# Optimization experiments

Measured on AMD Instinct MI355X. Metric: run time of the kernel, lower is better.

## Reference

```python
import jax, jax.numpy as jnp
import numpy as np

N, E, B, F, H = 50000, 600000, 256, 128, 128
RATIO = 0.8
BN_EPS = 1e-5


def _topk_keep(score, batch, mask):
    # Per-graph top-ceil(RATIO*live) selection, expressed as a fixed-size keep mask.
    s = jnp.where(mask, score, -jnp.inf)
    order = jnp.lexsort((-s, batch))  # primary: batch id, secondary: score desc
    rank = jnp.zeros(N, dtype=jnp.int32).at[order].set(jnp.arange(N, dtype=jnp.int32))
    total = jax.ops.segment_sum(jnp.ones(N, dtype=jnp.int32), batch, B)
    starts = jnp.cumsum(total) - total
    r_in_g = (rank - starts[batch]).astype(jnp.float32)  # rank within own graph
    live = jax.ops.segment_sum(mask.astype(jnp.float32), batch, B)
    k = jnp.ceil(RATIO * live)
    return (r_in_g < k[batch]) & mask


def _forward(x, edge_index, batch, W1s, b1s, W2s, b2s, gammas, betas, pool_ws):
    src, dst = edge_index[0], edge_index[1]
    mask = jnp.ones(N, dtype=bool)      # live-node mask (TopK pooling shrinks graphs)
    e_mask = jnp.ones(E, dtype=bool)    # live-edge mask
    out = jnp.zeros((B, 2 * H), dtype=x.dtype)
    for i in range(4):
        # GINConv (eps=0): MLP(x + sum_{j->i} x_j)
        msg = jnp.where(e_mask[:, None], x[src], 0.0)
        agg = jax.ops.segment_sum(msg, dst, num_segments=N)
        h = x + agg
        h = jax.nn.relu(h @ W1s[i] + b1s[i]) @ W2s[i] + b2s[i]
        # BatchNorm (training mode) over live nodes only
        m = mask[:, None].astype(h.dtype)
        n = jnp.maximum(jnp.sum(m), 1.0)
        mean = jnp.sum(h * m, axis=0) / n
        var = jnp.sum(((h - mean) ** 2) * m, axis=0) / n
        h = (h - mean) * jax.lax.rsqrt(var + BN_EPS) * gammas[i] + betas[i]
        h = jax.nn.relu(h) * m
        # TopKPooling(ratio=0.8): score = x@w/||w||, keep top-k per graph, scale by tanh
        w = pool_ws[i]
        score = (h @ w) / jnp.linalg.norm(w)
        keep = _topk_keep(score, batch, mask)
        x = jnp.where(keep[:, None], h * jnp.tanh(score)[:, None], 0.0)
        mask = keep
        e_mask = e_mask & keep[src] & keep[dst]
        # global max pool + global mean pool over live nodes
        mx = jax.ops.segment_max(jnp.where(mask[:, None], x, -jnp.inf), batch, num_segments=B)
        mx = jnp.where(jnp.isfinite(mx), mx, 0.0)
        cnt = jax.ops.segment_sum(mask.astype(x.dtype), batch, num_segments=B)
        mn = jax.ops.segment_sum(x, batch, num_segments=B) / jnp.maximum(cnt, 1.0)[:, None]
        out = out + jnp.concatenate([mx, mn], axis=1)  # x1 + x2 + x3 + x4
    return out


def setup_inputs() -> dict:
    key = jax.random.key(0)
    k = jax.random.split(key, 8)
    s = 1.0 / np.sqrt(H)
    return {
        "x": jax.random.normal(k[0], (N, F), jnp.float32),
        "edge_index": jax.random.randint(k[1], (2, E), 0, N),
        "batch": jnp.sort(jax.random.randint(k[2], (N,), 0, B)),
        "W1s": jax.random.normal(k[3], (4, F, H), jnp.float32) * s,
        "b1s": jax.random.normal(k[4], (4, H), jnp.float32) * s,
        "W2s": jax.random.normal(k[5], (4, H, H), jnp.float32) * s,
        "b2s": jax.random.normal(k[6], (4, H), jnp.float32) * s,
        "gammas": jnp.ones((4, H), jnp.float32),
        "betas": jnp.zeros((4, H), jnp.float32),
        "pool_ws": jax.random.normal(k[7], (4, H), jnp.float32) * s,
    }


def reference(x, edge_index, batch, W1s, b1s, W2s, b2s, gammas, betas, pool_ws):
    return _forward(x, edge_index, batch, W1s, b1s, W2s, b2s, gammas, betas, pool_ws)
```

## Files before the change

### kernel.cpp

```cpp
#include <hip/hip_runtime.h>
#include <hip/hip_bf16.h>
#include <math.h>


#define HF 128
#define CHUNK_LG 14

typedef __attribute__((ext_vector_type(8))) short short8;
typedef __attribute__((ext_vector_type(4))) float floatx4;

__device__ __forceinline__ unsigned short cvt_bf16(float f) {
    unsigned u = __float_as_uint(f);
    u = u + 0x7fffu + ((u >> 16) & 1u);
    return (unsigned short)(u >> 16);
}
__device__ __forceinline__ float bf16f(unsigned short h) {
    return __uint_as_float(((unsigned)h) << 16);
}

__device__ __forceinline__ void split3(float f, short& p1, short& p2, short& p3) {
    unsigned u = __float_as_uint(f);
    unsigned r = u + 0x7fffu + ((u >> 16) & 1u);
    p1 = (short)(r >> 16);
    float r1 = f - __uint_as_float(r & 0xffff0000u);
    unsigned u1 = __float_as_uint(r1);
    p2 = (short)(u1 >> 16);
    float r2 = r1 - __uint_as_float(u1 & 0xffff0000u);
    p3 = (short)(__float_as_uint(r2) >> 16);
}


__global__ __launch_bounds__(256)
void k_hist(const int* __restrict__ dst, unsigned int* __restrict__ partial,
            unsigned char* __restrict__ eslot, int* __restrict__ mask,
            float* __restrict__ stats4, float* __restrict__ out,
            int* __restrict__ lc,
            int N, int E, int nd4, int outsz, int X) {
    __shared__ unsigned int lh[12544];
    int bl = blockIdx.x, tid = threadIdx.x;
    for (int i = tid; i < nd4; i += 256) lh[i] = 0;
    __syncthreads();
    int e0 = bl << CHUNK_LG;
    int e1 = min(E, e0 + (1 << CHUNK_LG));
    for (int e = e0 + tid; e < e1; e += 256) {
        int d = dst[e];
        unsigned int old = atomicAdd(&lh[d >> 2], 1u << (8 * (d & 3)));
        eslot[e] = (unsigned char)((old >> (8 * (d & 3))) & 255u);
    }
    __syncthreads();
    for (int i = tid; i < nd4; i += 256) partial[(size_t)bl * nd4 + i] = lh[i];
    int gt = bl * 256 + tid, tot = X * 256;
    for (int i = gt; i < N; i += tot) mask[i] = 1;
    for (int i = gt; i < 4 * 256; i += tot) stats4[i] = 0.f;
    for (int i = gt; i < outsz; i += tot) out[i] = 0.f;
    if (gt < 5) lc[gt] = (gt == 0) ? N : 0;
}

__global__ __launch_bounds__(256)
void k_colsum(const unsigned int* __restrict__ partial, unsigned int* __restrict__ baseoff,
              int* __restrict__ deg, int* __restrict__ blocksum,
              int nd4, int X, int N) {
    __shared__ int red[256];
    int tid = threadIdx.x;
    int d4 = blockIdx.x * 256 + tid;
    unsigned int run = 0;
    if (d4 < nd4) {
        for (int bl = 0; bl < X; ++bl) {
            unsigned int c = partial[(size_t)bl * nd4 + d4];
            baseoff[(size_t)bl * nd4 + d4] = run;
            run += c;
        }
        int d = d4 * 4;
#pragma unroll
        for (int j = 0; j < 4; ++j)
            if (d + j < N) deg[d + j] = (int)((run >> (8 * j)) & 255u);
    }
    int tsum = (int)((run & 255u) + ((run >> 8) & 255u) + ((run >> 16) & 255u) + ((run >> 24) & 255u));
    red[tid] = tsum;
    __syncthreads();
    for (int off = 128; off; off >>= 1) {
        if (tid < off) red[tid] += red[tid + off];
        __syncthreads();
    }
    if (tid == 0) blocksum[blockIdx.x] = red[0];
}

__global__ void k_mid(const int* __restrict__ blocksum, int* __restrict__ blockoff,
                      int nblk, const int* __restrict__ batch,
                      int* __restrict__ gstart, int B, int n) {
    int t = threadIdx.x;
    if (t <= B) {
        int lo = 0, hi = n;
        while (lo < hi) { int mid = (lo + hi) >> 1; if (batch[mid] < t) lo = mid + 1; else hi = mid; }
        gstart[t] = lo;
    }
    if (t < 64) {
        int b0 = (t < nblk) ? blocksum[t] : 0;
        int v = b0;
#pragma unroll
        for (int off = 1; off < 64; off <<= 1) {
            int u = __shfl_up(v, off, 64);
            if (t >= off) v += u;
        }
        if (t < nblk) blockoff[t] = v - b0;
    }
}

__global__ __launch_bounds__(256)
void k_indptr(const int* __restrict__ deg, const int* __restrict__ blockoff,
              int* __restrict__ indptr, int nd4, int N) {
    __shared__ int ss[256];
    int tid = threadIdx.x;
    int d4 = blockIdx.x * 256 + tid;
    int dv[4] = {0, 0, 0, 0};
    int tsum = 0;
    if (d4 < nd4) {
        int d = d4 * 4;
#pragma unroll
        for (int j = 0; j < 4; ++j)
            if (d + j < N) { dv[j] = deg[d + j]; tsum += dv[j]; }
    }
    ss[tid] = tsum;
    __syncthreads();
    for (int off = 1; off < 256; off <<= 1) {
        int v = (tid >= off) ? ss[tid - off] : 0;
        __syncthreads();
        ss[tid] += v;
        __syncthreads();
    }
    if (d4 < nd4) {
        int b = blockoff[blockIdx.x] + ss[tid] - tsum;
        int d = d4 * 4;
#pragma unroll
        for (int j = 0; j < 4; ++j)
            if (d + j < N) { indptr[d + j] = b; b += dv[j]; }
        if (d4 == (N - 1) >> 2) indptr[N] = b;
    }
}

__global__ __launch_bounds__(256)
void k_place(const int* __restrict__ src, const int* __restrict__ dst,
             const unsigned char* __restrict__ eslot, const unsigned int* __restrict__ baseoff,
             const int* __restrict__ indptr, int* __restrict__ csr, int E, int nd4) {
    int e = blockIdx.x * 256 + threadIdx.x;
    if (e >= E) return;
    int d = dst[e];
    int bl = e >> CHUNK_LG;
    unsigned int bo = (baseoff[(size_t)bl * nd4 + (d >> 2)] >> (8 * (d & 3))) & 255u;
    csr[indptr[d] + (int)bo + (int)eslot[e]] = src[e];
}

__global__ void k_wsplit(const float* __restrict__ W1s, const float* __restrict__ W2s,
                         short8* __restrict__ wf) {
    int t = blockIdx.x * 256 + threadIdx.x;
    if (t >= 4 * 2 * 4 * 8 * 64) return;
    int lane = t & 63; int r = t >> 6;
    int ct = r & 7; r >>= 3; int kc = r & 3; r >>= 2; int g = r & 1; int l = r >> 1;
    const float* W = (g ? W2s : W1s) + l * 16384;
    int m = lane & 15, q = lane >> 4;
    int col = ct * 16 + m;
    short8 v1, v2, v3;
#pragma unroll
    for (int j = 0; j < 8; ++j) {
        float f = W[(size_t)(kc * 32 + q * 8 + j) * HF + col];
        unsigned short p1 = cvt_bf16(f); float r1 = f - bf16f(p1);
        unsigned short p2 = cvt_bf16(r1); float r2 = r1 - bf16f(p2);
        unsigned short p3 = cvt_bf16(r2);
        v1[j] = (short)p1; v2[j] = (short)p2; v3[j] = (short)p3;
    }
    size_t base = ((size_t)(l * 2 + g) * 6144) + ((size_t)(kc * 8 + ct) * 64) + lane;
    wf[base] = v1; wf[base + 2048] = v2; wf[base + 4096] = v3;
}


__global__ __launch_bounds__(256)
void k_agg(const float* __restrict__ x, const int* __restrict__ indptr,
           const int* __restrict__ csr, float* __restrict__ xa,
           const int* __restrict__ ll, const int* __restrict__ cnt, int N) {
    int widx = (blockIdx.x * 256 + threadIdx.x) >> 6;
    int count = ll ? *cnt : N;
    if (widx >= count) return;
    int wid = ll ? ll[widx] : widx;
    int lane = threadIdx.x & 63;
    int half = lane >> 5;
    int c = (lane & 31) * 4;
    int beg = indptr[wid], end = indptr[wid + 1];
    float4 a0 = make_float4(0.f, 0.f, 0.f, 0.f), a1 = a0, a2 = a0, a3 = a0;
    int e = beg + half;
    for (; e + 6 < end; e += 8) {
        int s0 = csr[e], s1 = csr[e + 2], s2 = csr[e + 4], s3 = csr[e + 6];
        float4 v0 = *(const float4*)&x[(size_t)s0 * HF + c];
        float4 v1 = *(const float4*)&x[(size_t)s1 * HF + c];
        float4 v2 = *(const float4*)&x[(size_t)s2 * HF + c];
        float4 v3 = *(const float4*)&x[(size_t)s3 * HF + c];
        a0.x += v0.x; a0.y += v0.y; a0.z += v0.z; a0.w += v0.w;
        a1.x += v1.x; a1.y += v1.y; a1.z += v1.z; a1.w += v1.w;
        a2.x += v2.x; a2.y += v2.y; a2.z += v2.z; a2.w += v2.w;
        a3.x += v3.x; a3.y += v3.y; a3.z += v3.z; a3.w += v3.w;
    }
    for (; e < end; e += 2) {
        int s0 = csr[e];
        float4 v0 = *(const float4*)&x[(size_t)s0 * HF + c];
        a0.x += v0.x; a0.y += v0.y; a0.z += v0.z; a0.w += v0.w;
    }
    float4 acc = make_float4(a0.x + a1.x + a2.x + a3.x, a0.y + a1.y + a2.y + a3.y,
                             a0.z + a1.z + a2.z + a3.z, a0.w + a1.w + a2.w + a3.w);
    acc.x += __shfl_down(acc.x, 32);
    acc.y += __shfl_down(acc.y, 32);
    acc.z += __shfl_down(acc.z, 32);
    acc.w += __shfl_down(acc.w, 32);
    if (half == 0) {
        float4 xv = *(const float4*)&x[(size_t)wid * HF + c];
        acc.x += xv.x; acc.y += xv.y; acc.z += xv.z; acc.w += xv.w;
        *(float4*)&xa[(size_t)wid * HF + c] = acc;
    }
}

__global__ __launch_bounds__(256, 2)
void k_mlp(const float* __restrict__ xa,
           const short8* __restrict__ wf1, const short8* __restrict__ wf2,
           const float* __restrict__ b1, const float* __restrict__ b2,
           const int* __restrict__ ll, const int* __restrict__ cnt,
           float* __restrict__ h, float* __restrict__ stats, int N) {
    __shared__ float sH[4 * 2 * 16 * 132];
    int tid = threadIdx.x;
    int count = ll ? *cnt : N;
    if (blockIdx.x * 128 >= count) return;
    int w = tid >> 6, lane = tid & 63;
    int m = lane & 15, q = lane >> 4;
    int base = blockIdx.x * 128 + w * 32;

    const float* aptr[2];
#pragma unroll
    for (int t = 0; t < 2; ++t) {
        int idx = base + t * 16 + m;
        int idc = (idx < count) ? idx : (count - 1);
        int row = ll ? ll[idc] : idc;
        aptr[t] = &xa[(size_t)row * HF + q * 8];
    }

    floatx4 acc[2][8];
#pragma unroll
    for (int t = 0; t < 2; ++t)
#pragma unroll
        for (int ct = 0; ct < 8; ++ct) acc[t][ct] = (floatx4){0.f, 0.f, 0.f, 0.f};

    float4 af0[2], af1[2];
#pragma unroll
    for (int t = 0; t < 2; ++t) {
        af0[t] = *(const float4*)(aptr[t]);
        af1[t] = *(const float4*)(aptr[t] + 4);
    }
#pragma unroll 1
    for (int kc = 0; kc < 4; ++kc) {
        short8 as[2][3];
#pragma unroll
        for (int t = 0; t < 2; ++t) {
            float av[8] = {af0[t].x, af0[t].y, af0[t].z, af0[t].w,
                           af1[t].x, af1[t].y, af1[t].z, af1[t].w};
#pragma unroll
            for (int j = 0; j < 8; ++j) {
                short p1, p2, p3;
                split3(av[j], p1, p2, p3);
                as[t][0][j] = p1; as[t][1][j] = p2; as[t][2][j] = p3;
            }
        }
        if (kc < 3) {
#pragma unroll
            for (int t = 0; t < 2; ++t) {
                af0[t] = *(const float4*)(aptr[t] + (kc + 1) * 32);
                af1[t] = *(const float4*)(aptr[t] + (kc + 1) * 32 + 4);
            }
        }
        const short8* bp = wf1 + (size_t)(kc * 8) * 64 + lane;
        short8 c1 = bp[0], c2 = bp[2048], c3 = bp[4096];
#pragma unroll
        for (int ct = 0; ct < 8; ++ct) {
            short8 n1, n2, n3;
            if (ct < 7) {
                const short8* np = bp + (size_t)(ct + 1) * 64;
                n1 = np[0]; n2 = np[2048]; n3 = np[4096];
            }
#pragma unroll
            for (int t = 0; t < 2; ++t) {
                acc[t][ct] = __builtin_amdgcn_mfma_f32_16x16x32_bf16(as[t][0], c1, acc[t][ct], 0, 0, 0);
                acc[t][ct] = __builtin_amdgcn_mfma_f32_16x16x32_bf16(as[t][1], c1, acc[t][ct], 0, 0, 0);
                acc[t][ct] = __builtin_amdgcn_mfma_f32_16x16x32_bf16(as[t][0], c2, acc[t][ct], 0, 0, 0);
                acc[t][ct] = __builtin_amdgcn_mfma_f32_16x16x32_bf16(as[t][2], c1, acc[t][ct], 0, 0, 0);
                acc[t][ct] = __builtin_amdgcn_mfma_f32_16x16x32_bf16(as[t][1], c2, acc[t][ct], 0, 0, 0);
                acc[t][ct] = __builtin_amdgcn_mfma_f32_16x16x32_bf16(as[t][0], c3, acc[t][ct], 0, 0, 0);
            }
            if (ct < 7) { c1 = n1; c2 = n2; c3 = n3; }
        }
    }

    float* sl[2] = {&sH[(w * 2) * 16 * 132], &sH[(w * 2 + 1) * 16 * 132]};
    float bb1[8];
#pragma unroll
    for (int ct = 0; ct < 8; ++ct) bb1[ct] = b1[ct * 16 + m];
#pragma unroll
    for (int t = 0; t < 2; ++t)
#pragma unroll
        for (int ct = 0; ct < 8; ++ct) {
#pragma unroll
            for (int reg = 0; reg < 4; ++reg) {
                float v = fmaxf(acc[t][ct][reg] + bb1[ct], 0.f);
                sl[t][(q * 4 + reg) * 132 + ct * 16 + m] = v;
            }
            acc[t][ct] = (floatx4){0.f, 0.f, 0.f, 0.f};
        }

#pragma unroll 1
    for (int kc = 0; kc < 4; ++kc) {
        short8 as[2][3];
#pragma unroll
        for (int t = 0; t < 2; ++t) {
            const float* ap = &sl[t][m * 132 + kc * 32 + q * 8];
            float4 x0 = *(const float4*)ap;
            float4 x1 = *(const float4*)(ap + 4);
            float av[8] = {x0.x, x0.y, x0.z, x0.w, x1.x, x1.y, x1.z, x1.w};
#pragma unroll
            for (int j = 0; j < 8; ++j) {
                short p1, p2, p3;
                split3(av[j], p1, p2, p3);
                as[t][0][j] = p1; as[t][1][j] = p2; as[t][2][j] = p3;
            }
        }
        const short8* bp = wf2 + (size_t)(kc * 8) * 64 + lane;
        short8 c1 = bp[0], c2 = bp[2048], c3 = bp[4096];
#pragma unroll
        for (int ct = 0; ct < 8; ++ct) {
            short8 n1, n2, n3;
            if (ct < 7) {
                const short8* np = bp + (size_t)(ct + 1) * 64;
                n1 = np[0]; n2 = np[2048]; n3 = np[4096];
            }
#pragma unroll
            for (int t = 0; t < 2; ++t) {
                acc[t][ct] = __builtin_amdgcn_mfma_f32_16x16x32_bf16(as[t][0], c1, acc[t][ct], 0, 0, 0);
                acc[t][ct] = __builtin_amdgcn_mfma_f32_16x16x32_bf16(as[t][1], c1, acc[t][ct], 0, 0, 0);
                acc[t][ct] = __builtin_amdgcn_mfma_f32_16x16x32_bf16(as[t][0], c2, acc[t][ct], 0, 0, 0);
                acc[t][ct] = __builtin_amdgcn_mfma_f32_16x16x32_bf16(as[t][2], c1, acc[t][ct], 0, 0, 0);
                acc[t][ct] = __builtin_amdgcn_mfma_f32_16x16x32_bf16(as[t][1], c2, acc[t][ct], 0, 0, 0);
                acc[t][ct] = __builtin_amdgcn_mfma_f32_16x16x32_bf16(as[t][0], c3, acc[t][ct], 0, 0, 0);
            }
            if (ct < 7) { c1 = n1; c2 = n2; c3 = n3; }
        }
    }

    float bb2[8];
#pragma unroll
    for (int ct = 0; ct < 8; ++ct) bb2[ct] = b2[ct * 16 + m];
    int rowv[2][4];
#pragma unroll
    for (int t = 0; t < 2; ++t)
#pragma unroll
        for (int reg = 0; reg < 4; ++reg) {
            int idx = base + t * 16 + q * 4 + reg;
            rowv[t][reg] = (idx < count) ? (ll ? ll[idx] : idx) : -1;
        }
    float sv[8], qv[8];
#pragma unroll
    for (int ct = 0; ct < 8; ++ct) {
        float s = 0.f, qq = 0.f;
#pragma unroll
        for (int t = 0; t < 2; ++t)
#pragma unroll
            for (int reg = 0; reg < 4; ++reg) {
                float v = acc[t][ct][reg] + bb2[ct];
                if (rowv[t][reg] >= 0) {
                    h[(size_t)rowv[t][reg] * HF + ct * 16 + m] = v;
                    s += v; qq += v * v;
                }
            }
        s += __shfl_xor(s, 16, 64);  s += __shfl_xor(s, 32, 64);
        qq += __shfl_xor(qq, 16, 64); qq += __shfl_xor(qq, 32, 64);
        sv[ct] = s; qv[ct] = qq;
    }
    __syncthreads();
    float* sStat = sH;
    if (lane < 16) {
#pragma unroll
        for (int ct = 0; ct < 8; ++ct) {
            sStat[w * 256 + ct * 16 + lane] = sv[ct];
            sStat[1024 + w * 256 + ct * 16 + lane] = qv[ct];
        }
    }
    __syncthreads();
    if (tid < 128) {
        float s = sStat[tid] + sStat[256 + tid] + sStat[512 + tid] + sStat[768 + tid];
        float qq = sStat[1024 + tid] + sStat[1280 + tid] + sStat[1536 + tid] + sStat[1792 + tid];
        atomicAdd(&stats[tid], s);
        atomicAdd(&stats[128 + tid], qq);
    }
}

__global__ __launch_bounds__(512)
void k_topkpool(const float* __restrict__ h, const float* __restrict__ stats,
                const float* __restrict__ gamma, const float* __restrict__ beta,
                const float* __restrict__ w, int* __restrict__ mask,
                const int* __restrict__ gstart, float* __restrict__ x,
                float* __restrict__ out, const int* __restrict__ cnt_in,
                int* __restrict__ ll_out, int* __restrict__ lcnt_out, int N) {
    __shared__ unsigned long long skey[512];
    __shared__ float sscore[512];
    __shared__ float sscale[128], sshift[128], swv[128], sred[128];
    __shared__ float smx[3 * 128], ssum[3 * 128];
    __shared__ int s_live, s_base;
    int b = blockIdx.x, tid = threadIdx.x;
    int gs = gstart[b], ge = gstart[b + 1];
    int size = ge - gs;
    if (size > 512) size = 512;
    int M = (size <= 256) ? 256 : 512;
    if (tid == 0) s_live = 0;
    if (tid < 128) { float wc = w[tid]; swv[tid] = wc; sred[tid] = wc * wc; }
    __syncthreads();
    for (int off = 64; off; off >>= 1) {
        if (tid < off) sred[tid] += sred[tid + off];
        __syncthreads();
    }
    float normv = sqrtf(sred[0]);
    if (tid < 128) {
        float n = fmaxf((float)(*cnt_in), 1.0f);
        float mean = stats[tid] / n;
        float var = fmaxf(stats[128 + tid] / n - mean * mean, 0.f);
        float sc = gamma[tid] * rsqrtf(var + 1e-5f);
        sscale[tid] = sc;
        sshift[tid] = beta[tid] - mean * sc;
    }
    __syncthreads();

    int wv = tid >> 6, lane = tid & 63;
    int lc = 0;
    for (int j = wv; j < M; j += 8) {
        unsigned long long key = (0xFFFFFFFFull << 32) | (unsigned)j;
        bool live = (j < size) && (mask[gs + j] != 0);
        if (live) {
            int c = lane * 2;
            float2 v = *(const float2*)&h[(size_t)(gs + j) * HF + c];
            float a0 = fmaxf(fmaf(v.x, sscale[c], sshift[c]), 0.f);
            float a1 = fmaxf(fmaf(v.y, sscale[c + 1], sshift[c + 1]), 0.f);
            float s = a0 * swv[c] + a1 * swv[c + 1];
#pragma unroll
            for (int off = 32; off; off >>= 1) s += __shfl_down(s, off, 64);
            if (lane == 0) {
                float scv = s / normv;
                sscore[j] = scv;
                unsigned u = __float_as_uint(scv);
                u = (u & 0x80000000u) ? ~u : (u | 0x80000000u);
                key = (((unsigned long long)(~u)) << 32) | (unsigned)j;
            }
        }
        if (lane == 0) { skey[j] = key; if (live) lc++; }
    }
    if (lane == 0 && lc) atomicAdd(&s_live, lc);
    __syncthreads();

    for (int k = 2; k <= M; k <<= 1) {
        for (int jj = k >> 1; jj > 0; jj >>= 1) {
            for (int t = tid; t < M; t += 512) {
                int ixj = t ^ jj;
                if (ixj > t) {
                    bool up = ((t & k) == 0);
                    unsigned long long A = skey[t], Bv = skey[ixj];
                    if ((A > Bv) == up) { skey[t] = Bv; skey[ixj] = A; }
                }
            }
            __syncthreads();
        }
    }
    int live = s_live;
    int kk = (live > 0) ? (int)ceilf(0.8f * (float)live) : 0;

    if (tid == 0 && ll_out) s_base = atomicAdd(lcnt_out, kk);
    for (int j = tid; j < size; j += 512) sscore[j] = tanhf(sscore[j]);
    __syncthreads();
    if (ll_out) {
        for (int p = tid; p < kk; p += 512)
            ll_out[s_base + p] = gs + (int)(skey[p] & 0xFFFFFFFFu);
    }

    int f = tid & 127, hf = tid >> 7;
    float mx = -INFINITY, sum = 0.f;
    for (int p = hf; p < live; p += 4) {
        int local = (int)(skey[p] & 0xFFFFFFFFu);
        int node = gs + local;
        float v = 0.f;
        bool keep = (p < kk);
        if (keep) {
            float hv = h[(size_t)node * HF + f];
            hv = fmaxf(fmaf(hv, sscale[f], sshift[f]), 0.f);
            v = hv * sscore[local];
            mx = fmaxf(mx, v);
            sum += v;
        }
        x[(size_t)node * HF + f] = v;
        if (f == 0) mask[node] = keep ? 1 : 0;
    }
    if (hf) { smx[(hf - 1) * 128 + f] = mx; ssum[(hf - 1) * 128 + f] = sum; }
    __syncthreads();
    if (hf == 0) {
#pragma unroll
        for (int k2 = 0; k2 < 3; ++k2) {
            mx = fmaxf(mx, smx[k2 * 128 + f]);
            sum += ssum[k2 * 128 + f];
        }
        float mxo = (kk > 0) ? mx : 0.f;
        float mn = sum / (float)(kk > 0 ? kk : 1);
        out[b * 256 + f] += mxo;
        out[b * 256 + 128 + f] += mn;
    }
}


extern "C" void kernel_launch(void* const* d_in, const int* in_sizes, int n_in,
                              void* d_out, int out_size, void* d_ws, size_t ws_size,
                              hipStream_t stream) {
    const float* x_in    = (const float*)d_in[0];
    const int*   ei      = (const int*)d_in[1];
    const int*   batch   = (const int*)d_in[2];
    const float* W1s     = (const float*)d_in[3];
    const float* b1s     = (const float*)d_in[4];
    const float* W2s     = (const float*)d_in[5];
    const float* b2s     = (const float*)d_in[6];
    const float* gammas  = (const float*)d_in[7];
    const float* betas   = (const float*)d_in[8];
    const float* pool_ws = (const float*)d_in[9];

    int N = in_sizes[0] / HF;
    int E = in_sizes[1] / 2;
    int B = out_size / (2 * HF);
    const int* src = ei;
    const int* dst = ei + E;
    int nd4 = (N + 3) >> 2;
    int X = (E + (1 << CHUNK_LG) - 1) >> CHUNK_LG;
    int nblk = (nd4 + 255) >> 8;

    char* ws = (char*)d_ws;
    size_t off = 0;
    auto alloc = [&](size_t bytes) -> void* {
        void* p = ws + off;
        off = (off + bytes + 255) & ~(size_t)255;
        return p;
    };
    float* xa      = (float*)alloc((size_t)N * HF * 4);
    float* h       = (float*)alloc((size_t)N * HF * 4);
    float* xbuf    = (float*)alloc((size_t)N * HF * 4);
    int*   mask    = (int*)alloc((size_t)N * 4);
    int*   deg     = (int*)alloc((size_t)(N + 1) * 4);
    int*   indptr  = (int*)alloc((size_t)(N + 1) * 4);
    int*   csr     = (int*)alloc((size_t)E * 4);
    int*   gstart  = (int*)alloc((size_t)(B + 1) * 4);
    float* stats4  = (float*)alloc(4 * 256 * 4);
    int*   lc      = (int*)alloc(8 * 4);
    int*   llA     = (int*)alloc((size_t)N * 4);
    int*   llB     = (int*)alloc((size_t)N * 4);
    int*   blocksum = (int*)alloc(64 * 4);
    int*   blockoff = (int*)alloc(64 * 4);
    short8* wfrag  = (short8*)alloc((size_t)8 * 6144 * 16);
    unsigned int* partial = (unsigned int*)alloc((size_t)X * nd4 * 4);
    unsigned int* baseoff = (unsigned int*)alloc((size_t)X * nd4 * 4);
    unsigned char* eslot  = (unsigned char*)alloc((size_t)E);
    float* out    = (float*)d_out;

    int tb = 256;
    k_hist<<<X, tb, 0, stream>>>(dst, partial, eslot, mask, stats4, out, lc,
                                 N, E, nd4, out_size, X);
    k_wsplit<<<64, tb, 0, stream>>>(W1s, W2s, wfrag);
    k_colsum<<<nblk, tb, 0, stream>>>(partial, baseoff, deg, blocksum, nd4, X, N);
    k_mid<<<1, 512, 0, stream>>>(blocksum, blockoff, nblk, batch, gstart, B, N);
    k_indptr<<<nblk, tb, 0, stream>>>(deg, blockoff, indptr, nd4, N);
    k_place<<<(E + tb - 1) / tb, tb, 0, stream>>>(src, dst, eslot, baseoff, indptr, csr, E, nd4);

    int bound[4];
    bound[0] = N;
    for (int i = 1; i < 4; ++i) bound[i] = (4 * bound[i - 1] + 4) / 5 + B;

    const int* ll_in[4] = {nullptr, llA, llB, llA};
    int*       ll_ot[4] = {llA, llB, llA, llB};

    for (int i = 0; i < 4; ++i) {
        const float* xc = (i == 0) ? x_in : xbuf;
        float* stats = stats4 + i * 256;
        k_agg<<<(bound[i] + 3) / 4, tb, 0, stream>>>(xc, indptr, csr, xa,
                                                     ll_in[i], lc + i, N);
        k_mlp<<<(bound[i] + 127) / 128, tb, 0, stream>>>(xa,
                                                wfrag + (size_t)(i * 2) * 6144,
                                                wfrag + (size_t)(i * 2 + 1) * 6144,
                                                b1s + i * 128, b2s + i * 128,
                                                ll_in[i], lc + i, h, stats, N);
        k_topkpool<<<B, 512, 0, stream>>>(h, stats, gammas + i * 128, betas + i * 128,
                                          pool_ws + i * 128, mask, gstart, xbuf, out,
                                          lc + i, ll_ot[i], lc + i + 1, N);
    }
}
```

Measured before the change: 582.2 us.

## Split pooling into a node-parallel score kernel and a live-list top-k kernel

Moves the BatchNorm, ReLU, score and tanh-scaled x computation out of the per-graph top-k kernel into a separate node-parallel kernel that visits only live nodes. The top-k kernel then sorts over each graph's compacted live segment (gseg), with a bitonic size rounded up to a power of two from 32, and writes zeros for the dropped nodes. The global mask array and its initialisation go away. Pool-weight norms are precomputed once in k_mid. The intent is to spread the elementwise work across all CUs instead of B blocks and to shrink the sorts as graphs shrink, at the cost of one extra launch and an extra x round trip.

```diff
diff --git a/kernel.cpp b/kernel.cpp
--- a/kernel.cpp
+++ b/kernel.cpp
@@ -32,7 +32,7 @@
 
 __global__ __launch_bounds__(256)
 void k_hist(const int* __restrict__ dst, unsigned int* __restrict__ partial,
-            unsigned char* __restrict__ eslot, int* __restrict__ mask,
+            unsigned char* __restrict__ eslot,
             float* __restrict__ stats4, float* __restrict__ out,
             int* __restrict__ lc,
             int N, int E, int nd4, int outsz, int X) {
@@ -50,7 +50,6 @@
     __syncthreads();
     for (int i = tid; i < nd4; i += 256) partial[(size_t)bl * nd4 + i] = lh[i];
     int gt = bl * 256 + tid, tot = X * 256;
-    for (int i = gt; i < N; i += tot) mask[i] = 1;
     for (int i = gt; i < 4 * 256; i += tot) stats4[i] = 0.f;
     for (int i = gt; i < outsz; i += tot) out[i] = 0.f;
     if (gt < 5) lc[gt] = (gt == 0) ? N : 0;
@@ -87,12 +86,19 @@
 
 __global__ void k_mid(const int* __restrict__ blocksum, int* __restrict__ blockoff,
                       int nblk, const int* __restrict__ batch,
-                      int* __restrict__ gstart, int B, int n) {
+                      int* __restrict__ gstart, int B, int n,
+                      const float* __restrict__ pw, float* __restrict__ normv4) {
     int t = threadIdx.x;
     if (t <= B) {
         int lo = 0, hi = n;
         while (lo < hi) { int mid = (lo + hi) >> 1; if (batch[mid] < t) lo = mid + 1; else hi = mid; }
         gstart[t] = lo;
+    }
+    if (t >= 508) {
+        int l = t - 508;
+        float s = 0.f;
+        for (int j = 0; j < HF; ++j) { float wv = pw[l * HF + j]; s += wv * wv; }
+        normv4[l] = sqrtf(s);
     }
     if (t < 64) {
         int b0 = (t < nblk) ? blocksum[t] : 0;
@@ -395,70 +401,70 @@
     }
 }
 
-__global__ __launch_bounds__(512)
-void k_topkpool(const float* __restrict__ h, const float* __restrict__ stats,
-                const float* __restrict__ gamma, const float* __restrict__ beta,
-                const float* __restrict__ w, int* __restrict__ mask,
-                const int* __restrict__ gstart, float* __restrict__ x,
-                float* __restrict__ out, const int* __restrict__ cnt_in,
-                int* __restrict__ ll_out, int* __restrict__ lcnt_out, int N) {
+__global__ __launch_bounds__(256)
+void k_score(const float* __restrict__ h, const float* __restrict__ stats,
+             const float* __restrict__ gamma, const float* __restrict__ beta,
+             const float* __restrict__ w, const float* __restrict__ normv,
+             const int* __restrict__ ll, const int* __restrict__ cnt,
+             float* __restrict__ score, float* __restrict__ x, int N) {
+    int widx = (blockIdx.x * 256 + threadIdx.x) >> 6;
+    int count = ll ? *cnt : N;
+    if (widx >= count) return;
+    int node = ll ? ll[widx] : widx;
+    int lane = threadIdx.x & 63;
+    int c = lane * 2;
+    float n = fmaxf((float)count, 1.0f);
+    float su0 = stats[c], su1 = stats[c + 1];
+    float sq0 = stats[128 + c], sq1 = stats[128 + c + 1];
+    float m0 = su0 / n, m1 = su1 / n;
+    float va0 = fmaxf(sq0 / n - m0 * m0, 0.f);
+    float va1 = fmaxf(sq1 / n - m1 * m1, 0.f);
+    float sc0 = gamma[c] * rsqrtf(va0 + 1e-5f);
+    float sc1 = gamma[c + 1] * rsqrtf(va1 + 1e-5f);
+    float sh0 = beta[c] - m0 * sc0;
+    float sh1 = beta[c + 1] - m1 * sc1;
+    float2 hv = *(const float2*)&h[(size_t)node * HF + c];
+    float a0 = fmaxf(fmaf(hv.x, sc0, sh0), 0.f);
+    float a1 = fmaxf(fmaf(hv.y, sc1, sh1), 0.f);
+    float s = a0 * w[c] + a1 * w[c + 1];
+#pragma unroll
+    for (int off = 1; off < 64; off <<= 1) s += __shfl_xor(s, off, 64);
+    float scv = s / normv[0];
+    if (lane == 0) score[node] = scv;
+    float t = tanhf(scv);
+    *(float2*)&x[(size_t)node * HF + c] = make_float2(a0 * t, a1 * t);
+}
+
+__global__ __launch_bounds__(1024)
+void k_topkpool(const float* __restrict__ score, const int* __restrict__ ll_in,
+                const int* __restrict__ gstart, const int* __restrict__ gseg_in,
+                int* __restrict__ ll_out, int* __restrict__ gseg_out,
+                int* __restrict__ lcnt_out, float* __restrict__ x,
+                float* __restrict__ out) {
     __shared__ unsigned long long skey[512];
-    __shared__ float sscore[512];
-    __shared__ float sscale[128], sshift[128], swv[128], sred[128];
-    __shared__ float smx[3 * 128], ssum[3 * 128];
-    __shared__ int s_live, s_base;
+    __shared__ float smx[7 * 128], ssum[7 * 128];
+    __shared__ int s_base;
     int b = blockIdx.x, tid = threadIdx.x;
-    int gs = gstart[b], ge = gstart[b + 1];
-    int size = ge - gs;
-    if (size > 512) size = 512;
-    int M = (size <= 256) ? 256 : 512;
-    if (tid == 0) s_live = 0;
-    if (tid < 128) { float wc = w[tid]; swv[tid] = wc; sred[tid] = wc * wc; }
-    __syncthreads();
-    for (int off = 64; off; off >>= 1) {
-        if (tid < off) sred[tid] += sred[tid + off];
-        __syncthreads();
-    }
-    float normv = sqrtf(sred[0]);
-    if (tid < 128) {
-        float n = fmaxf((float)(*cnt_in), 1.0f);
-        float mean = stats[tid] / n;
-        float var = fmaxf(stats[128 + tid] / n - mean * mean, 0.f);
-        float sc = gamma[tid] * rsqrtf(var + 1e-5f);
-        sscale[tid] = sc;
-        sshift[tid] = beta[tid] - mean * sc;
-    }
-    __syncthreads();
-
-    int wv = tid >> 6, lane = tid & 63;
-    int lc = 0;
-    for (int j = wv; j < M; j += 8) {
-        unsigned long long key = (0xFFFFFFFFull << 32) | (unsigned)j;
-        bool live = (j < size) && (mask[gs + j] != 0);
-        if (live) {
-            int c = lane * 2;
-            float2 v = *(const float2*)&h[(size_t)(gs + j) * HF + c];
-            float a0 = fmaxf(fmaf(v.x, sscale[c], sshift[c]), 0.f);
-            float a1 = fmaxf(fmaf(v.y, sscale[c + 1], sshift[c + 1]), 0.f);
-            float s = a0 * swv[c] + a1 * swv[c + 1];
-#pragma unroll
-            for (int off = 32; off; off >>= 1) s += __shfl_down(s, off, 64);
-            if (lane == 0) {
-                float scv = s / normv;
-                sscore[j] = scv;
-                unsigned u = __float_as_uint(scv);
-                u = (u & 0x80000000u) ? ~u : (u | 0x80000000u);
-                key = (((unsigned long long)(~u)) << 32) | (unsigned)j;
-            }
-        }
-        if (lane == 0) { skey[j] = key; if (live) lc++; }
-    }
-    if (lane == 0 && lc) atomicAdd(&s_live, lc);
-    __syncthreads();
-
+    int s0, lv;
+    if (ll_in) { s0 = gseg_in[2 * b]; lv = gseg_in[2 * b + 1]; }
+    else { s0 = gstart[b]; lv = gstart[b + 1] - s0; }
+    if (lv > 512) lv = 512;
+    int M = 32; while (M < lv) M <<= 1;
+
+    for (int p = tid; p < M; p += 1024) {
+        unsigned long long key = ~0ull;
+        if (p < lv) {
+            int node = ll_in ? ll_in[s0 + p] : (s0 + p);
+            unsigned u = __float_as_uint(score[node]);
+            u = (u & 0x80000000u) ? ~u : (u | 0x80000000u);
+            key = (((unsigned long long)(~u)) << 32) | (unsigned)node;
+        }
+        skey[p] = key;
+    }
+    __syncthreads();
     for (int k = 2; k <= M; k <<= 1) {
         for (int jj = k >> 1; jj > 0; jj >>= 1) {
-            for (int t = tid; t < M; t += 512) {
+            for (int t = tid; t < M; t += 1024) {
                 int ixj = t ^ jj;
                 if (ixj > t) {
                     bool up = ((t & k) == 0);
@@ -469,39 +475,33 @@
             __syncthreads();
         }
     }
-    int live = s_live;
-    int kk = (live > 0) ? (int)ceilf(0.8f * (float)live) : 0;
-
-    if (tid == 0 && ll_out) s_base = atomicAdd(lcnt_out, kk);
-    for (int j = tid; j < size; j += 512) sscore[j] = tanhf(sscore[j]);
-    __syncthreads();
-    if (ll_out) {
-        for (int p = tid; p < kk; p += 512)
-            ll_out[s_base + p] = gs + (int)(skey[p] & 0xFFFFFFFFu);
-    }
-
-    int f = tid & 127, hf = tid >> 7;
+    int kk = (lv > 0) ? (int)ceilf(0.8f * (float)lv) : 0;
+    if (tid == 0) s_base = atomicAdd(lcnt_out, kk);
+    __syncthreads();
+    int sb = s_base;
+    if (tid == 0) { gseg_out[2 * b] = sb; gseg_out[2 * b + 1] = kk; }
+    for (int p = tid; p < kk; p += 1024)
+        ll_out[sb + p] = (int)(skey[p] & 0xFFFFFFFFu);
+
+    int wv = tid >> 6, lane = tid & 63;
+    for (int p = kk + wv; p < lv; p += 16) {
+        int node = (int)(skey[p] & 0xFFFFFFFFu);
+        *(float2*)&x[(size_t)node * HF + lane * 2] = make_float2(0.f, 0.f);
+    }
+
+    int f = tid & 127, g = tid >> 7;
     float mx = -INFINITY, sum = 0.f;
-    for (int p = hf; p < live; p += 4) {
-        int local = (int)(skey[p] & 0xFFFFFFFFu);
-        int node = gs + local;
-        float v = 0.f;
-        bool keep = (p < kk);
-        if (keep) {
-            float hv = h[(size_t)node * HF + f];
-            hv = fmaxf(fmaf(hv, sscale[f], sshift[f]), 0.f);
-            v = hv * sscore[local];
-            mx = fmaxf(mx, v);
-            sum += v;
-        }
-        x[(size_t)node * HF + f] = v;
-        if (f == 0) mask[node] = keep ? 1 : 0;
-    }
-    if (hf) { smx[(hf - 1) * 128 + f] = mx; ssum[(hf - 1) * 128 + f] = sum; }
-    __syncthreads();
-    if (hf == 0) {
-#pragma unroll
-        for (int k2 = 0; k2 < 3; ++k2) {
+    for (int p = g; p < kk; p += 8) {
+        int node = (int)(skey[p] & 0xFFFFFFFFu);
+        float v = x[(size_t)node * HF + f];
+        mx = fmaxf(mx, v);
+        sum += v;
+    }
+    if (g) { smx[(g - 1) * 128 + f] = mx; ssum[(g - 1) * 128 + f] = sum; }
+    __syncthreads();
+    if (g == 0) {
+#pragma unroll
+        for (int k2 = 0; k2 < 7; ++k2) {
             mx = fmaxf(mx, smx[k2 * 128 + f]);
             sum += ssum[k2 * 128 + f];
         }
@@ -546,15 +546,18 @@
     float* xa      = (float*)alloc((size_t)N * HF * 4);
     float* h       = (float*)alloc((size_t)N * HF * 4);
     float* xbuf    = (float*)alloc((size_t)N * HF * 4);
-    int*   mask    = (int*)alloc((size_t)N * 4);
+    float* score   = (float*)alloc((size_t)N * 4);
     int*   deg     = (int*)alloc((size_t)(N + 1) * 4);
     int*   indptr  = (int*)alloc((size_t)(N + 1) * 4);
     int*   csr     = (int*)alloc((size_t)E * 4);
     int*   gstart  = (int*)alloc((size_t)(B + 1) * 4);
     float* stats4  = (float*)alloc(4 * 256 * 4);
+    float* normv4  = (float*)alloc(4 * 4);
     int*   lc      = (int*)alloc(8 * 4);
     int*   llA     = (int*)alloc((size_t)N * 4);
     int*   llB     = (int*)alloc((size_t)N * 4);
+    int*   gsegA   = (int*)alloc((size_t)2 * B * 4);
+    int*   gsegB   = (int*)alloc((size_t)2 * B * 4);
     int*   blocksum = (int*)alloc(64 * 4);
     int*   blockoff = (int*)alloc(64 * 4);
     short8* wfrag  = (short8*)alloc((size_t)8 * 6144 * 16);
@@ -564,11 +567,12 @@
     float* out    = (float*)d_out;
 
     int tb = 256;
-    k_hist<<<X, tb, 0, stream>>>(dst, partial, eslot, mask, stats4, out, lc,
+    k_hist<<<X, tb, 0, stream>>>(dst, partial, eslot, stats4, out, lc,
                                  N, E, nd4, out_size, X);
     k_wsplit<<<64, tb, 0, stream>>>(W1s, W2s, wfrag);
     k_colsum<<<nblk, tb, 0, stream>>>(partial, baseoff, deg, blocksum, nd4, X, N);
-    k_mid<<<1, 512, 0, stream>>>(blocksum, blockoff, nblk, batch, gstart, B, N);
+    k_mid<<<1, 512, 0, stream>>>(blocksum, blockoff, nblk, batch, gstart, B, N,
+                                 pool_ws, normv4);
     k_indptr<<<nblk, tb, 0, stream>>>(deg, blockoff, indptr, nd4, N);
     k_place<<<(E + tb - 1) / tb, tb, 0, stream>>>(src, dst, eslot, baseoff, indptr, csr, E, nd4);
 
@@ -576,8 +580,10 @@
     bound[0] = N;
     for (int i = 1; i < 4; ++i) bound[i] = (4 * bound[i - 1] + 4) / 5 + B;
 
-    const int* ll_in[4] = {nullptr, llA, llB, llA};
-    int*       ll_ot[4] = {llA, llB, llA, llB};
+    const int* ll_in[4]   = {nullptr, llA, llB, llA};
+    int*       ll_ot[4]   = {llA, llB, llA, llB};
+    const int* gseg_in[4] = {nullptr, gsegA, gsegB, gsegA};
+    int*       gseg_ot[4] = {gsegA, gsegB, gsegA, gsegB};
 
     for (int i = 0; i < 4; ++i) {
         const float* xc = (i == 0) ? x_in : xbuf;
@@ -589,8 +595,12 @@
                                                 wfrag + (size_t)(i * 2 + 1) * 6144,
                                                 b1s + i * 128, b2s + i * 128,
                                                 ll_in[i], lc + i, h, stats, N);
-        k_topkpool<<<B, 512, 0, stream>>>(h, stats, gammas + i * 128, betas + i * 128,
-                                          pool_ws + i * 128, mask, gstart, xbuf, out,
-                                          lc + i, ll_ot[i], lc + i + 1, N);
-    }
-}
+        k_score<<<(bound[i] + 3) / 4, tb, 0, stream>>>(h, stats, gammas + i * 128,
+                                                betas + i * 128, pool_ws + i * 128,
+                                                normv4 + i, ll_in[i], lc + i,
+                                                score, xbuf, N);
+        k_topkpool<<<B, 1024, 0, stream>>>(score, ll_in[i], gstart, gseg_in[i],
+                                           ll_ot[i], gseg_ot[i], lc + i + 1,
+                                           xbuf, out);
+    }
+}
```

After: 526.3 us. -9.6%, faster.
